# Performance work log

Hardware: AMD Instinct MI355X
Metric: run time of the kernel (lower is better)

The kernel has to match this reference:

```python
import jax, jax.numpy as jnp
import numpy as np

B, DIN, HID, DOUT, E, TOPK = 8192, 1024, 2048, 1024, 8, 2
GHID = HID // 2  # gating hidden


def setup_inputs() -> dict:
    key = jax.random.key(0)
    ks = jax.random.split(key, 16)
    s = lambda fan_in: 1.0 / np.sqrt(fan_in)
    return {
        "x": jax.random.normal(ks[0], (B, DIN), dtype=jnp.float32),
        # stacked expert params, leading axis = expert
        "w1": jax.random.uniform(ks[1], (E, DIN, HID), jnp.float32, -s(DIN), s(DIN)),
        "b1": jax.random.uniform(ks[2], (E, HID), jnp.float32, -s(DIN), s(DIN)),
        "w2": jax.random.uniform(ks[3], (E, HID, HID), jnp.float32, -s(HID), s(HID)),
        "b2": jax.random.uniform(ks[4], (E, HID), jnp.float32, -s(HID), s(HID)),
        "w3": jax.random.uniform(ks[5], (E, HID, DOUT), jnp.float32, -s(HID), s(HID)),
        "b3": jax.random.uniform(ks[6], (E, DOUT), jnp.float32, -s(HID), s(HID)),
        "wp": jax.random.uniform(ks[7], (E, DIN, HID), jnp.float32, -s(DIN), s(DIN)),
        "bp": jax.random.uniform(ks[8], (E, HID), jnp.float32, -s(DIN), s(DIN)),
        # gating network: Linear(DIN, GHID) -> ReLU -> Linear(GHID, E)
        "gw1": jax.random.uniform(ks[9], (DIN, GHID), jnp.float32, -s(DIN), s(DIN)),
        "gb1": jax.random.uniform(ks[10], (GHID,), jnp.float32, -s(DIN), s(DIN)),
        "gw2": jax.random.uniform(ks[11], (GHID, E), jnp.float32, -s(GHID), s(GHID)),
        "gb2": jax.random.uniform(ks[12], (E,), jnp.float32, -s(GHID), s(GHID)),
    }


def reference(x, w1, b1, w2, b2, w3, b3, wp, bp, gw1, gb1, gw2, gb2):
    # gating: [B, E]
    gate_logits = jnp.maximum(x @ gw1 + gb1, 0.0) @ gw2 + gb2
    topk_w, topk_i = jax.lax.top_k(gate_logits, TOPK)  # [B, K]
    topk_w = jax.nn.softmax(topk_w, axis=1)
    # dense per-expert residual MLP (dropout is identity in eval mode)
    h = jnp.maximum(jnp.einsum('bi,eih->beh', x, w1) + b1, 0.0)  # [B,E,HID]
    out = jnp.einsum('beh,ehg->beg', h, w2) + b2                  # [B,E,HID]
    identity = jnp.einsum('bi,eih->beh', x, wp) + bp              # projection
    out = jnp.maximum(out + identity, 0.0)
    expert_out = jnp.einsum('beh,eho->beo', out, w3) + b3         # [B,E,DOUT]
    # scatter top-k weights into dense [B, E] gate
    gate = jnp.zeros_like(gate_logits).at[jnp.arange(x.shape[0])[:, None], topk_i].set(topk_w)
    return jnp.einsum('beo,be->bo', expert_out, gate)             # [B, DOUT]
```

## Files before the change

### kernel.cpp

```cpp
#include <hip/hip_runtime.h>
#include <hip/hip_bf16.h>
#include <cstdint>
#include <cstddef>

#define TOK  8192
#define DIN  1024
#define HID  2048
#define DOUTN 1024
#define NEXP 8
#define GHID 1024

typedef __attribute__((ext_vector_type(8))) short bf16x8;
typedef __attribute__((ext_vector_type(4))) float floatx4;
typedef __attribute__((ext_vector_type(8))) unsigned short ushort8v;

__device__ __forceinline__ unsigned short f2b(float f) {
  unsigned int u = __float_as_uint(f);
  u += 0x7fffu + ((u >> 16) & 1u);
  return (unsigned short)(u >> 16);
}

__device__ __forceinline__ float b2f(unsigned short b) {
  return __uint_as_float(((unsigned int)b) << 16);
}

__device__ __forceinline__ void async_cp16(const unsigned short* g, char* lds) {
  __builtin_amdgcn_global_load_lds(
      (const __attribute__((address_space(1))) unsigned int*)g,
      (__attribute__((address_space(3))) unsigned int*)lds, 16, 0, 0);
}


__global__ void cvt_x_kernel(const float* __restrict__ src,
                             unsigned short* __restrict__ xb,
                             unsigned short* __restrict__ xcat, int n4) {
  int i = blockIdx.x * blockDim.x + threadIdx.x;
  if (i >= n4) return;
  float4 v = ((const float4*)src)[i];
  ushort4 hi, lo;
  hi.x = f2b(v.x); lo.x = f2b(v.x - b2f(hi.x));
  hi.y = f2b(v.y); lo.y = f2b(v.y - b2f(hi.y));
  hi.z = f2b(v.z); lo.z = f2b(v.z - b2f(hi.z));
  hi.w = f2b(v.w); lo.w = f2b(v.w - b2f(hi.w));
  ((ushort4*)xb)[i] = hi;
  int t = i >> 8;
  int kk = i & 255;
  ushort4* rowc = (ushort4*)(xcat + (size_t)t * 3072);
  rowc[kk] = hi;
  rowc[256 + kk] = hi;
  rowc[512 + kk] = lo;
}

__global__ void cvt_transpose_v2(const float* __restrict__ src,
                                 unsigned short* __restrict__ dst, int N,
                                 long sEstride, long dEstride, int ldDst) {
  __shared__ __align__(16) unsigned short t[64][72];
  long e = blockIdx.z;
  src += e * sEstride;
  dst += e * dEstride;
  int n0 = blockIdx.x * 64, k0 = blockIdx.y * 64;
  int tid = threadIdx.x;
  int kr = tid >> 2, qc = tid & 3;
  const float* s = src + (long)(k0 + kr) * N + n0 + qc * 16;
#pragma unroll
  for (int i = 0; i < 4; i++) {
    float4 v = *(const float4*)(s + i * 4);
    int nn = qc * 16 + i * 4;
    t[nn + 0][kr] = f2b(v.x);
    t[nn + 1][kr] = f2b(v.y);
    t[nn + 2][kr] = f2b(v.z);
    t[nn + 3][kr] = f2b(v.w);
  }
  __syncthreads();
  int c = tid & 7;
  int nr = tid >> 3;
#pragma unroll
  for (int p = 0; p < 2; p++) {
    int n = nr + 32 * p;
    ushort8v v = *(const ushort8v*)&t[n][c * 8];
    *(ushort8v*)(dst + (long)(n0 + n) * ldDst + k0 + c * 8) = v;
  }
}

__global__ void cvt_gw1_kernel(const float* __restrict__ src,
                               unsigned short* __restrict__ dst) {
  __shared__ float tile[32][33];
  int n0 = blockIdx.x * 32, k0 = blockIdx.y * 32;
  int x = threadIdx.x, y = threadIdx.y;
#pragma unroll
  for (int i = 0; i < 4; i++)
    tile[y + 8 * i][x] = src[(long)(k0 + y + 8 * i) * GHID + n0 + x];
  __syncthreads();
#pragma unroll
  for (int i = 0; i < 4; i++) {
    float v = tile[x][y + 8 * i];
    unsigned short hi = f2b(v);
    unsigned short lo = f2b(v - b2f(hi));
    size_t r = (size_t)(n0 + y + 8 * i) * 3072 + k0 + x;
    dst[r] = hi;
    dst[r + 1024] = lo;
    dst[r + 2048] = hi;
  }
}


#define KLOOP(pa0, pa1, pb0, pb1, NKT)                                        \
  for (int kt = 0; kt < (NKT); ++kt) {                                        \
    __syncthreads();                                                          \
    async_cp16((pa0) + kt * 32, ldsA0);                                       \
    async_cp16((pa1) + kt * 32, ldsA0 + 4096);                                \
    async_cp16((pb0) + kt * 32, ldsB0);                                       \
    async_cp16((pb1) + kt * 32, ldsB0 + 4096);                                \
    __syncthreads();                                                          \
    bf16x8 af[4], bfr[4];                                                     \
    _Pragma("unroll") for (int i = 0; i < 4; i++) {                           \
      af[i] = *(const bf16x8*)(AsB + i * 1024);                               \
      bfr[i] = *(const bf16x8*)(BsB + i * 1024);                              \
    }                                                                         \
    _Pragma("unroll") for (int mi = 0; mi < 4; mi++)                          \
      _Pragma("unroll") for (int ni = 0; ni < 4; ni++)                        \
        acc[mi][ni] = __builtin_amdgcn_mfma_f32_16x16x32_bf16(                \
            af[mi], bfr[ni], acc[mi][ni], 0, 0, 0);                           \
  }

#define TILE_SETUP()                                                          \
  int tid = threadIdx.x;                                                      \
  int sr = tid >> 2;                                                          \
  int lchunk = (tid & 3) ^ ((sr >> 1) & 3);                                   \
  int koffA = lchunk * 8;                                                     \
  char* ldsA0 = (char*)As + (tid & 192) * 16;                                 \
  char* ldsB0 = (char*)Bs + (tid & 192) * 16;                                 \
  int lane = tid & 63, wv = tid >> 6;                                         \
  int wm = (wv >> 1) << 6, wn = (wv & 1) << 6;                                \
  int q = lane >> 4, l15 = lane & 15;                                         \
  int abase = l15 * 64 + ((q ^ ((l15 >> 1) & 3)) << 4);                       \
  const char* AsB = (const char*)As + wm * 64 + abase;                        \
  const char* BsB = (const char*)Bs + wn * 64 + abase;                        \
  floatx4 acc[4][4] = {};


__global__ __launch_bounds__(256, 4) void gating_mfma(
    const unsigned short* __restrict__ xcat,
    const unsigned short* __restrict__ gw1t3,
    const float* __restrict__ gb1, float* __restrict__ H) {
  __shared__ __align__(16) unsigned short As[128 * 32];
  __shared__ __align__(16) unsigned short Bs[128 * 32];
  TILE_SETUP();
  int row0 = blockIdx.y << 7, tn = blockIdx.x << 7;

  const unsigned short* a0p = xcat + (size_t)(row0 + sr) * 3072 + koffA;
  const unsigned short* a1p = xcat + (size_t)(row0 + 64 + sr) * 3072 + koffA;
  const unsigned short* b0p = gw1t3 + (size_t)(tn + sr) * 3072 + koffA;
  const unsigned short* b1p = gw1t3 + (size_t)(tn + 64 + sr) * 3072 + koffA;

  KLOOP(a0p, a1p, b0p, b1p, 3072 / 32);

  int crow = row0 + wm + q * 4;
  int ccol0 = tn + wn + l15;
#pragma unroll
  for (int ni = 0; ni < 4; ++ni) {
    int col = ccol0 + ni * 16;
    float bias = gb1[col];
#pragma unroll
    for (int mi = 0; mi < 4; ++mi)
#pragma unroll
      for (int rg = 0; rg < 4; ++rg) {
        int rr = crow + mi * 16 + rg;
        H[(size_t)rr * GHID + col] = fmaxf(acc[mi][ni][rg] + bias, 0.f);
      }
  }
}


__global__ void gating2_topk(const float* __restrict__ H,
                             const float* __restrict__ gw2,
                             const float* __restrict__ gb2,
                             int* __restrict__ gidx, float* __restrict__ gwt) {
  int wv = threadIdx.x >> 6, lane = threadIdx.x & 63;
  int t = blockIdx.x * 4 + wv;
  const float* hrow = H + (size_t)t * GHID;
  float acc[8] = {};
  for (int k = lane; k < GHID; k += 64) {
    float v = hrow[k];
    float4 g0 = *(const float4*)(gw2 + (size_t)k * 8);
    float4 g1 = *(const float4*)(gw2 + (size_t)k * 8 + 4);
    acc[0] += v * g0.x; acc[1] += v * g0.y; acc[2] += v * g0.z; acc[3] += v * g0.w;
    acc[4] += v * g1.x; acc[5] += v * g1.y; acc[6] += v * g1.z; acc[7] += v * g1.w;
  }
#pragma unroll
  for (int off = 32; off > 0; off >>= 1)
#pragma unroll
    for (int e = 0; e < 8; e++) acc[e] += __shfl_xor(acc[e], off);

  if (lane == 0) {
    float l[8];
#pragma unroll
    for (int e = 0; e < 8; e++) l[e] = acc[e] + gb2[e];
    int b0 = 0; float v0 = l[0];
#pragma unroll
    for (int e = 1; e < 8; e++) if (l[e] > v0) { v0 = l[e]; b0 = e; }
    int b1 = -1; float v1 = -3.4e38f;
#pragma unroll
    for (int e = 0; e < 8; e++)
      if (e != b0 && l[e] > v1) { v1 = l[e]; b1 = e; }
    float ex = expf(v1 - v0);
    float inv = 1.f / (1.f + ex);
    gidx[2 * t] = b0; gidx[2 * t + 1] = b1;
    gwt[2 * t] = inv; gwt[2 * t + 1] = ex * inv;
  }
}


__global__ void route_count(const int* __restrict__ gidx, int* cnt) {
  int t = blockIdx.x * blockDim.x + threadIdx.x;
  int lane = threadIdx.x & 63;
  int e0 = gidx[2 * t], e1 = gidx[2 * t + 1];
#pragma unroll 1
  for (int e = 0; e < NEXP; e++) {
    unsigned long long m0 = __ballot(e0 == e);
    if (m0 && lane == __ffsll(m0) - 1) atomicAdd(&cnt[e], (int)__popcll(m0));
    unsigned long long m1 = __ballot(e1 == e);
    if (m1 && lane == __ffsll(m1) - 1) atomicAdd(&cnt[e], (int)__popcll(m1));
  }
}

__global__ void route_scan(const int* __restrict__ cnt, int* base_, int* cur) {
  if (threadIdx.x == 0) {
    int s = 0;
    for (int e = 0; e < NEXP; e++) { base_[e] = s; cur[e] = s; s += cnt[e]; }
  }
}

__global__ void route_scatter(const int* __restrict__ gidx,
                              const float* __restrict__ gwt, int* cur,
                              int* __restrict__ rt, float* __restrict__ rw,
                              int* __restrict__ inv) {
  int t = blockIdx.x * blockDim.x + threadIdx.x;
  int lane = threadIdx.x & 63;
  int e0 = gidx[2 * t], e1 = gidx[2 * t + 1];
  float w0 = gwt[2 * t], w1 = gwt[2 * t + 1];
#pragma unroll 1
  for (int e = 0; e < NEXP; e++) {
#pragma unroll 1
    for (int s = 0; s < 2; s++) {
      int mye = s ? e1 : e0;
      unsigned long long m = __ballot(mye == e);
      if (m) {
        int leader = __ffsll(m) - 1;
        int bb = 0;
        if (lane == leader) bb = atomicAdd(&cur[e], (int)__popcll(m));
        bb = __shfl(bb, leader);
        if (mye == e) {
          int pos = bb + (int)__popcll(m & ((1ull << lane) - 1ull));
          rt[pos] = t;
          rw[pos] = s ? w1 : w0;
          inv[2 * t + s] = pos;
        }
      }
    }
  }
}

__global__ void xgather_kernel(const unsigned short* __restrict__ xb,
                               const int* __restrict__ rt,
                               unsigned short* __restrict__ hx) {
  int slot = blockIdx.x;
  int c = threadIdx.x;
  int t = rt[slot];
  ((ushort8v*)(hx + (size_t)slot * 3072 + 2048))[c] =
      ((const ushort8v*)(xb + (size_t)t * 1024))[c];
}

__global__ void combine_kernel(const float* __restrict__ s3,
                               const int* __restrict__ inv,
                               float* __restrict__ out) {
  int t = blockIdx.x;
  int c = threadIdx.x;
  const float4* r0 = (const float4*)(s3 + (size_t)inv[2 * t] * DOUTN);
  const float4* r1 = (const float4*)(s3 + (size_t)inv[2 * t + 1] * DOUTN);
  float4 a = r0[c], b = r1[c];
  float4 o = {a.x + b.x, a.y + b.y, a.z + b.z, a.w + b.w};
  ((float4*)(out + (size_t)t * DOUTN))[c] = o;
}


#define STG_AU(dst, u, ktI)                                                   \
  async_cp16(Abase + aOff[u] + (size_t)(ktI) * 64, (dst) + (u) * 8192 + wvb)
#define STG_BU(dst, u, ktI)                                                   \
  async_cp16(Bbase + bOff[u] + (size_t)(ktI) * 64, (dst) + (u) * 8192 + wvb)

#define LDA8(dst, baseA, h)                                                   \
  _Pragma("unroll") for (int mi = 0; mi < 4; ++mi)                            \
      _Pragma("unroll") for (int kk = 0; kk < 2; ++kk)                        \
          (dst)[mi * 2 + kk] = *(const bf16x8*)(                              \
              (baseA) + ((wmo + (h)*64 + mi * 16 + l15) * 128 +               \
                         ((s0 ^ (kk << 2)) * 16)));

#define LDB4(dst, baseB, ch)                                                  \
  _Pragma("unroll") for (int ni = 0; ni < 2; ++ni)                            \
      _Pragma("unroll") for (int kk = 0; kk < 2; ++kk)                        \
          (dst)[ni * 2 + kk] = *(const bf16x8*)(                              \
              (baseB) + ((wno + (ch)*32 + ni * 16 + l15) * 128 +              \
                         ((s0 ^ (kk << 2)) * 16)));

#define MM8(aF, bF, mo, no)                                                   \
  _Pragma("unroll") for (int mi = 0; mi < 4; ++mi)                            \
      _Pragma("unroll") for (int ni = 0; ni < 2; ++ni)                        \
          _Pragma("unroll") for (int kk = 0; kk < 2; ++kk)                    \
              acc[(mo) + mi][(no) + ni] =                                     \
                  __builtin_amdgcn_mfma_f32_16x16x32_bf16(                    \
                      (aF)[mi * 2 + kk], (bF)[ni * 2 + kk],                   \
                      acc[(mo) + mi][(no) + ni], 0, 0, 0);


template <int MODE>
__global__ __launch_bounds__(512, 2) void moe_gemm8(
    const unsigned short* __restrict__ hx, const unsigned short* __restrict__ obuf,
    const unsigned short* __restrict__ w1t, const unsigned short* __restrict__ w2p,
    const unsigned short* __restrict__ w3t, const float* __restrict__ b1,
    const float* __restrict__ b2, const float* __restrict__ bp,
    const float* __restrict__ b3, const float* __restrict__ rw,
    const int* __restrict__ cnt, const int* __restrict__ basep,
    unsigned short* __restrict__ hxout, unsigned short* __restrict__ oout,
    float* __restrict__ s3) {
  __shared__ __align__(16) char smem[131072];

  const int gx = (int)gridDim.x;
  const int nwg = gx * (int)gridDim.y;
  int orig = (int)blockIdx.y * gx + (int)blockIdx.x;
  int q8 = nwg >> 3, r8 = nwg & 7;
  int xcd = orig & 7, loc = orig >> 3;
  int wg = (xcd < r8 ? xcd * (q8 + 1) : r8 * (q8 + 1) + (xcd - r8) * q8) + loc;
  int bx = wg % gx, by = wg / gx;

  int lt = by;
  int e, cn = 0, ok = 0;
  for (e = 0; e < NEXP; ++e) {
    int c = cnt[e];
    int nt = (c + 255) >> 8;
    if (lt < nt) { cn = c; ok = 1; break; }
    lt -= nt;
  }
  if (!ok) return;
  const int be = basep[e];
  const int row0 = lt << 8;
  const int tn = bx << 8;
  const int cnm1 = cn - 1;

  const int tid = threadIdx.x;
  const int lane = tid & 63, wv = tid >> 6;
  const int wmo = (wv >> 2) * 128;
  const int wno = (wv & 3) * 64;
  const int q = lane >> 4, l15 = lane & 15;
  const int s0 = q ^ (l15 & 7);
  const int wvb = wv * 1024;
  const int srow = tid >> 3;
  const int skoff = ((tid & 7) ^ (srow & 7)) * 8;

  const unsigned short* Abase;
  const unsigned short* Bbase;
  size_t strideA, strideB;
  if (MODE == 1) {
    Abase = hx + 2048; strideA = 3072;
    Bbase = w1t + (size_t)e * HID * DIN; strideB = DIN;
  } else if (MODE == 2) {
    Abase = hx; strideA = 3072;
    Bbase = w2p + (size_t)e * HID * 3072; strideB = 3072;
  } else {
    Abase = obuf; strideA = HID;
    Bbase = w3t + (size_t)e * DOUTN * HID; strideB = HID;
  }
  const int NT = (MODE == 1) ? (DIN / 64) : (MODE == 2 ? (3072 / 64) : (HID / 64));

  size_t aOff[4], bOff[4];
#pragma unroll
  for (int u = 0; u < 4; ++u) {
    int ra = min(row0 + u * 64 + srow, cnm1);
    aOff[u] = (size_t)(be + ra) * strideA + skoff;
    bOff[u] = (size_t)(tn + u * 64 + srow) * strideB + skoff;
  }

  char* const A0s = smem;
  char* const B0s = smem + 32768;
  char* const A1s = smem + 65536;
  char* const B1s = smem + 98304;

  floatx4 acc[8][4] = {};
  bf16x8 a[8], bA[4], bB[4];

  STG_AU(A0s, 0, 0); STG_AU(A0s, 1, 0); STG_AU(A0s, 2, 0); STG_AU(A0s, 3, 0);
  STG_BU(B0s, 0, 0); STG_BU(B0s, 1, 0); STG_BU(B0s, 2, 0); STG_BU(B0s, 3, 0);
  asm volatile("s_waitcnt vmcnt(4)" ::: "memory");
  STG_AU(A1s, 0, 1); STG_AU(A1s, 2, 1);
  STG_BU(B1s, 0, 1); STG_BU(B1s, 1, 1);
  STG_AU(A1s, 1, 1); STG_AU(A1s, 3, 1);
  asm volatile("s_waitcnt vmcnt(6)" ::: "memory");
  __builtin_amdgcn_s_barrier();

  for (int t = 0; t < NT; ++t) {
    char* const curA = (t & 1) ? A1s : A0s;
    char* const curB = (t & 1) ? B1s : B0s;
    char* const nxtB = (t & 1) ? B0s : B1s;
    LDA8(a, curA, 0);
    LDB4(bA, curB, 0);
    if (t + 1 < NT) { STG_BU(nxtB, 2, t + 1); STG_BU(nxtB, 3, t + 1); }
    __builtin_amdgcn_s_barrier();
    asm volatile("s_waitcnt lgkmcnt(0)" ::: "memory");
    __builtin_amdgcn_s_setprio(1);
    MM8(a, bA, 0, 0);
    __builtin_amdgcn_s_setprio(0);
    __builtin_amdgcn_s_barrier();
    LDB4(bB, curB, 1);
    if (t + 2 < NT) { STG_AU(curA, 0, t + 2); STG_AU(curA, 2, t + 2); }
    __builtin_amdgcn_s_barrier();
    asm volatile("s_waitcnt lgkmcnt(0)" ::: "memory");
    __builtin_amdgcn_s_setprio(1);
    MM8(a, bB, 0, 2);
    __builtin_amdgcn_s_setprio(0);
    __builtin_amdgcn_s_barrier();
    LDA8(a, curA, 1);
    if (t + 2 < NT) { STG_BU(curB, 0, t + 2); STG_BU(curB, 1, t + 2); }
    __builtin_amdgcn_s_barrier();
    asm volatile("s_waitcnt lgkmcnt(0)" ::: "memory");
    __builtin_amdgcn_s_setprio(1);
    MM8(a, bB, 4, 2);
    __builtin_amdgcn_s_setprio(0);
    __builtin_amdgcn_s_barrier();
    if (t + 2 < NT) {
      STG_AU(curA, 1, t + 2); STG_AU(curA, 3, t + 2);
      __builtin_amdgcn_s_setprio(1);
      MM8(a, bA, 4, 0);
      __builtin_amdgcn_s_setprio(0);
      asm volatile("s_waitcnt vmcnt(6)" ::: "memory");
    } else {
      __builtin_amdgcn_s_setprio(1);
      MM8(a, bA, 4, 0);
      __builtin_amdgcn_s_setprio(0);
      asm volatile("s_waitcnt vmcnt(0)" ::: "memory");
    }
    __builtin_amdgcn_s_barrier();
  }

  const int crow = row0 + wmo + q * 4;
  const int ccol0 = tn + wno + l15;
  if (MODE == 1) {
    const float* bb = b1 + (size_t)e * HID;
    float bias[4];
#pragma unroll
    for (int ni = 0; ni < 4; ++ni) bias[ni] = bb[ccol0 + ni * 16];
#pragma unroll
    for (int mi = 0; mi < 8; ++mi)
#pragma unroll
      for (int rg = 0; rg < 4; ++rg) {
        int rr = crow + mi * 16 + rg;
        if (rr < cn) {
#pragma unroll
          for (int ni = 0; ni < 4; ++ni)
            hxout[(size_t)(be + rr) * 3072 + ccol0 + ni * 16] =
                f2b(fmaxf(acc[mi][ni][rg] + bias[ni], 0.f));
        }
      }
  } else if (MODE == 2) {
    const float* bb = b2 + (size_t)e * HID;
    const float* bq = bp + (size_t)e * HID;
    float bias[4];
#pragma unroll
    for (int ni = 0; ni < 4; ++ni)
      bias[ni] = bb[ccol0 + ni * 16] + bq[ccol0 + ni * 16];
#pragma unroll
    for (int mi = 0; mi < 8; ++mi)
#pragma unroll
      for (int rg = 0; rg < 4; ++rg) {
        int rr = crow + mi * 16 + rg;
        if (rr < cn) {
#pragma unroll
          for (int ni = 0; ni < 4; ++ni)
            oout[(size_t)(be + rr) * HID + ccol0 + ni * 16] =
                f2b(fmaxf(acc[mi][ni][rg] + bias[ni], 0.f));
        }
      }
  } else {
    const float* bb = b3 + (size_t)e * DOUTN;
    float bias[4];
#pragma unroll
    for (int ni = 0; ni < 4; ++ni) bias[ni] = bb[ccol0 + ni * 16];
#pragma unroll
    for (int mi = 0; mi < 8; ++mi)
#pragma unroll
      for (int rg = 0; rg < 4; ++rg) {
        int rr = crow + mi * 16 + rg;
        if (rr < cn) {
          float wgt = rw[be + rr];
#pragma unroll
          for (int ni = 0; ni < 4; ++ni)
            s3[(size_t)(be + rr) * DOUTN + ccol0 + ni * 16] =
                (acc[mi][ni][rg] + bias[ni]) * wgt;
        }
      }
  }
}


extern "C" void kernel_launch(void* const* d_in, const int* in_sizes, int n_in,
                              void* d_out, int out_size, void* d_ws,
                              size_t ws_size, hipStream_t stream) {
  const float* x = (const float*)d_in[0];
  const float* w1 = (const float*)d_in[1];
  const float* b1 = (const float*)d_in[2];
  const float* w2 = (const float*)d_in[3];
  const float* b2 = (const float*)d_in[4];
  const float* w3 = (const float*)d_in[5];
  const float* b3 = (const float*)d_in[6];
  const float* wp = (const float*)d_in[7];
  const float* bp = (const float*)d_in[8];
  const float* gw1 = (const float*)d_in[9];
  const float* gb1 = (const float*)d_in[10];
  const float* gw2 = (const float*)d_in[11];
  const float* gb2 = (const float*)d_in[12];
  float* outp = (float*)d_out;
  char* ws = (char*)d_ws;

  const size_t o_w2p = 0;
  const size_t o_w3t = o_w2p + (size_t)NEXP * HID * 3072 * 2;
  const size_t o_xb  = o_w3t + (size_t)NEXP * DOUTN * HID * 2;
  const size_t o_w1t = o_xb + (size_t)TOK * DIN * 2;
  const size_t o_hg  = o_w1t + (size_t)NEXP * HID * DIN * 2;
  const size_t o_hx  = o_hg + (size_t)TOK * GHID * 4;
  const size_t o_gw1t3 = o_hx + (size_t)2 * TOK * 3072 * 2;
  const size_t o_gidx = o_gw1t3 + (size_t)GHID * 3072 * 2;
  const size_t o_gw  = o_gidx + (size_t)2 * TOK * 4;
  const size_t o_cnt = o_gw + (size_t)2 * TOK * 4;
  const size_t o_base = o_cnt + 128;
  const size_t o_cur = o_base + 128;
  const size_t o_rt  = o_cur + 128;
  const size_t o_rw  = o_rt + (size_t)2 * TOK * 4;
  const size_t o_inv = o_rw + (size_t)2 * TOK * 4;
  const size_t o_xcat = o_hx;
  const size_t o_ob   = o_w1t;
  const size_t o_s3   = o_w2p;

  unsigned short* w2p = (unsigned short*)(ws + o_w2p);
  unsigned short* w3t = (unsigned short*)(ws + o_w3t);
  unsigned short* xb = (unsigned short*)(ws + o_xb);
  unsigned short* w1t = (unsigned short*)(ws + o_w1t);
  float* hg = (float*)(ws + o_hg);
  unsigned short* hx = (unsigned short*)(ws + o_hx);
  unsigned short* gw1t3 = (unsigned short*)(ws + o_gw1t3);
  unsigned short* xcat = (unsigned short*)(ws + o_xcat);
  unsigned short* obuf = (unsigned short*)(ws + o_ob);
  float* s3 = (float*)(ws + o_s3);
  int* gidx = (int*)(ws + o_gidx);
  float* gwt = (float*)(ws + o_gw);
  int* cnt = (int*)(ws + o_cnt);
  int* basep = (int*)(ws + o_base);
  int* cur = (int*)(ws + o_cur);
  int* rtl = (int*)(ws + o_rt);
  float* rwl = (float*)(ws + o_rw);
  int* invp = (int*)(ws + o_inv);

  hipMemsetAsync(ws + o_cnt, 0, 32, stream);

  cvt_x_kernel<<<dim3(TOK * DIN / 4 / 256), 256, 0, stream>>>(x, xb, xcat, TOK * DIN / 4);
  cvt_gw1_kernel<<<dim3(GHID / 32, DIN / 32), dim3(32, 8), 0, stream>>>(gw1, gw1t3);
  cvt_transpose_v2<<<dim3(HID / 64, DIN / 64, NEXP), 256, 0, stream>>>(
      w1, w1t, HID, (long)DIN * HID, (long)HID * DIN, DIN);
  cvt_transpose_v2<<<dim3(HID / 64, HID / 64, NEXP), 256, 0, stream>>>(
      w2, w2p, HID, (long)HID * HID, (long)HID * 3072, 3072);
  cvt_transpose_v2<<<dim3(HID / 64, DIN / 64, NEXP), 256, 0, stream>>>(
      wp, w2p + 2048, HID, (long)DIN * HID, (long)HID * 3072, 3072);
  cvt_transpose_v2<<<dim3(DOUTN / 64, HID / 64, NEXP), 256, 0, stream>>>(
      w3, w3t, DOUTN, (long)HID * DOUTN, (long)DOUTN * HID, HID);

  gating_mfma<<<dim3(GHID / 128, TOK / 128), 256, 0, stream>>>(xcat, gw1t3, gb1, hg);
  gating2_topk<<<dim3(TOK / 4), 256, 0, stream>>>(hg, gw2, gb2, gidx, gwt);
  route_count<<<dim3(TOK / 256), 256, 0, stream>>>(gidx, cnt);
  route_scan<<<1, 64, 0, stream>>>(cnt, basep, cur);
  route_scatter<<<dim3(TOK / 256), 256, 0, stream>>>(gidx, gwt, cur, rtl, rwl, invp);
  xgather_kernel<<<dim3(2 * TOK), 128, 0, stream>>>(xb, rtl, hx);

  moe_gemm8<1><<<dim3(HID / 256, 71), 512, 0, stream>>>(
      hx, obuf, w1t, w2p, w3t, b1, b2, bp, b3, rwl, cnt, basep, hx, obuf, s3);
  moe_gemm8<2><<<dim3(HID / 256, 71), 512, 0, stream>>>(
      hx, obuf, w1t, w2p, w3t, b1, b2, bp, b3, rwl, cnt, basep, hx, obuf, s3);
  moe_gemm8<3><<<dim3(DOUTN / 256, 71), 512, 0, stream>>>(
      hx, obuf, w1t, w2p, w3t, b1, b2, bp, b3, rwl, cnt, basep, hx, obuf, s3);

  combine_kernel<<<dim3(TOK), 256, 0, stream>>>(s3, invp, outp);
}
```

Before: 1.033 ms.

## Route gating GEMM through moe_gemm8 with split-K and split-K the final expert GEMM

Removes the separate 128x128 gating GEMM kernel and runs the gating first layer through the larger 256x256 moe_gemm8 tile path (new MODE 0), split into two K halves whose partial sums are written to separate buffers. Bias and ReLU are moved into gating2_topk, which now sums the two partials. The third expert GEMM (MODE 3) is also split-K by two to add more workgroups, with the second partial added in combine_kernel. In exchange there is extra fp32 partial-buffer traffic and more buffer aliasing in the workspace.

```diff
diff --git a/kernel.cpp b/kernel.cpp
--- a/kernel.cpp
+++ b/kernel.cpp
@@ -104,84 +104,19 @@
 }
 
 
-#define KLOOP(pa0, pa1, pb0, pb1, NKT)                                        \
-  for (int kt = 0; kt < (NKT); ++kt) {                                        \
-    __syncthreads();                                                          \
-    async_cp16((pa0) + kt * 32, ldsA0);                                       \
-    async_cp16((pa1) + kt * 32, ldsA0 + 4096);                                \
-    async_cp16((pb0) + kt * 32, ldsB0);                                       \
-    async_cp16((pb1) + kt * 32, ldsB0 + 4096);                                \
-    __syncthreads();                                                          \
-    bf16x8 af[4], bfr[4];                                                     \
-    _Pragma("unroll") for (int i = 0; i < 4; i++) {                           \
-      af[i] = *(const bf16x8*)(AsB + i * 1024);                               \
-      bfr[i] = *(const bf16x8*)(BsB + i * 1024);                              \
-    }                                                                         \
-    _Pragma("unroll") for (int mi = 0; mi < 4; mi++)                          \
-      _Pragma("unroll") for (int ni = 0; ni < 4; ni++)                        \
-        acc[mi][ni] = __builtin_amdgcn_mfma_f32_16x16x32_bf16(                \
-            af[mi], bfr[ni], acc[mi][ni], 0, 0, 0);                           \
-  }
-
-#define TILE_SETUP()                                                          \
-  int tid = threadIdx.x;                                                      \
-  int sr = tid >> 2;                                                          \
-  int lchunk = (tid & 3) ^ ((sr >> 1) & 3);                                   \
-  int koffA = lchunk * 8;                                                     \
-  char* ldsA0 = (char*)As + (tid & 192) * 16;                                 \
-  char* ldsB0 = (char*)Bs + (tid & 192) * 16;                                 \
-  int lane = tid & 63, wv = tid >> 6;                                         \
-  int wm = (wv >> 1) << 6, wn = (wv & 1) << 6;                                \
-  int q = lane >> 4, l15 = lane & 15;                                         \
-  int abase = l15 * 64 + ((q ^ ((l15 >> 1) & 3)) << 4);                       \
-  const char* AsB = (const char*)As + wm * 64 + abase;                        \
-  const char* BsB = (const char*)Bs + wn * 64 + abase;                        \
-  floatx4 acc[4][4] = {};
-
-
-__global__ __launch_bounds__(256, 4) void gating_mfma(
-    const unsigned short* __restrict__ xcat,
-    const unsigned short* __restrict__ gw1t3,
-    const float* __restrict__ gb1, float* __restrict__ H) {
-  __shared__ __align__(16) unsigned short As[128 * 32];
-  __shared__ __align__(16) unsigned short Bs[128 * 32];
-  TILE_SETUP();
-  int row0 = blockIdx.y << 7, tn = blockIdx.x << 7;
-
-  const unsigned short* a0p = xcat + (size_t)(row0 + sr) * 3072 + koffA;
-  const unsigned short* a1p = xcat + (size_t)(row0 + 64 + sr) * 3072 + koffA;
-  const unsigned short* b0p = gw1t3 + (size_t)(tn + sr) * 3072 + koffA;
-  const unsigned short* b1p = gw1t3 + (size_t)(tn + 64 + sr) * 3072 + koffA;
-
-  KLOOP(a0p, a1p, b0p, b1p, 3072 / 32);
-
-  int crow = row0 + wm + q * 4;
-  int ccol0 = tn + wn + l15;
-#pragma unroll
-  for (int ni = 0; ni < 4; ++ni) {
-    int col = ccol0 + ni * 16;
-    float bias = gb1[col];
-#pragma unroll
-    for (int mi = 0; mi < 4; ++mi)
-#pragma unroll
-      for (int rg = 0; rg < 4; ++rg) {
-        int rr = crow + mi * 16 + rg;
-        H[(size_t)rr * GHID + col] = fmaxf(acc[mi][ni][rg] + bias, 0.f);
-      }
-  }
-}
-
-
-__global__ void gating2_topk(const float* __restrict__ H,
+__global__ void gating2_topk(const float* __restrict__ H0,
+                             const float* __restrict__ H1,
+                             const float* __restrict__ gb1,
                              const float* __restrict__ gw2,
                              const float* __restrict__ gb2,
                              int* __restrict__ gidx, float* __restrict__ gwt) {
   int wv = threadIdx.x >> 6, lane = threadIdx.x & 63;
   int t = blockIdx.x * 4 + wv;
-  const float* hrow = H + (size_t)t * GHID;
+  const float* h0 = H0 + (size_t)t * GHID;
+  const float* h1 = H1 + (size_t)t * GHID;
   float acc[8] = {};
   for (int k = lane; k < GHID; k += 64) {
-    float v = hrow[k];
+    float v = fmaxf(h0[k] + h1[k] + gb1[k], 0.f);
     float4 g0 = *(const float4*)(gw2 + (size_t)k * 8);
     float4 g1 = *(const float4*)(gw2 + (size_t)k * 8 + 4);
     acc[0] += v * g0.x; acc[1] += v * g0.y; acc[2] += v * g0.z; acc[3] += v * g0.w;
@@ -272,14 +207,18 @@
 }
 
 __global__ void combine_kernel(const float* __restrict__ s3,
+                               const float* __restrict__ s3b,
                                const int* __restrict__ inv,
                                float* __restrict__ out) {
   int t = blockIdx.x;
   int c = threadIdx.x;
-  const float4* r0 = (const float4*)(s3 + (size_t)inv[2 * t] * DOUTN);
-  const float4* r1 = (const float4*)(s3 + (size_t)inv[2 * t + 1] * DOUTN);
-  float4 a = r0[c], b = r1[c];
-  float4 o = {a.x + b.x, a.y + b.y, a.z + b.z, a.w + b.w};
+  int i0 = inv[2 * t], i1 = inv[2 * t + 1];
+  float4 a = ((const float4*)(s3 + (size_t)i0 * DOUTN))[c];
+  float4 b = ((const float4*)(s3 + (size_t)i1 * DOUTN))[c];
+  float4 a2 = ((const float4*)(s3b + (size_t)i0 * DOUTN))[c];
+  float4 b2 = ((const float4*)(s3b + (size_t)i1 * DOUTN))[c];
+  float4 o = {a.x + b.x + a2.x + b2.x, a.y + b.y + a2.y + b2.y,
+              a.z + b.z + a2.z + b2.z, a.w + b.w + a2.w + b2.w};
   ((float4*)(out + (size_t)t * DOUTN))[c] = o;
 }
 
@@ -312,38 +251,43 @@
                       (aF)[mi * 2 + kk], (bF)[ni * 2 + kk],                   \
                       acc[(mo) + mi][(no) + ni], 0, 0, 0);
 
-
 template <int MODE>
 __global__ __launch_bounds__(512, 2) void moe_gemm8(
     const unsigned short* __restrict__ hx, const unsigned short* __restrict__ obuf,
     const unsigned short* __restrict__ w1t, const unsigned short* __restrict__ w2p,
-    const unsigned short* __restrict__ w3t, const float* __restrict__ b1,
+    const unsigned short* __restrict__ w3t, const unsigned short* __restrict__ xcat,
+    const unsigned short* __restrict__ gw1t3, const float* __restrict__ b1,
     const float* __restrict__ b2, const float* __restrict__ bp,
     const float* __restrict__ b3, const float* __restrict__ rw,
     const int* __restrict__ cnt, const int* __restrict__ basep,
     unsigned short* __restrict__ hxout, unsigned short* __restrict__ oout,
-    float* __restrict__ s3) {
+    float* __restrict__ s3, float* __restrict__ s3b,
+    float* __restrict__ hg0, float* __restrict__ hg1) {
   __shared__ __align__(16) char smem[131072];
 
-  const int gx = (int)gridDim.x;
-  const int nwg = gx * (int)gridDim.y;
+  const int gx = (int)gridDim.x, gy = (int)gridDim.y;
+  const int kz = (int)blockIdx.z;
+  const int nwg = gx * gy;
   int orig = (int)blockIdx.y * gx + (int)blockIdx.x;
   int q8 = nwg >> 3, r8 = nwg & 7;
   int xcd = orig & 7, loc = orig >> 3;
   int wg = (xcd < r8 ? xcd * (q8 + 1) : r8 * (q8 + 1) + (xcd - r8) * q8) + loc;
-  int bx = wg % gx, by = wg / gx;
-
-  int lt = by;
-  int e, cn = 0, ok = 0;
-  for (e = 0; e < NEXP; ++e) {
-    int c = cnt[e];
-    int nt = (c + 255) >> 8;
-    if (lt < nt) { cn = c; ok = 1; break; }
-    lt -= nt;
-  }
-  if (!ok) return;
-  const int be = basep[e];
-  const int row0 = lt << 8;
+  int by = wg % gy, bx = wg / gy;
+
+  int e = 0, cn = TOK, be = 0, row0 = by << 8;
+  if (MODE != 0) {
+    int lt = by, ok = 0;
+    cn = 0;
+    for (e = 0; e < NEXP; ++e) {
+      int c = cnt[e];
+      int nt = (c + 255) >> 8;
+      if (lt < nt) { cn = c; ok = 1; break; }
+      lt -= nt;
+    }
+    if (!ok) return;
+    be = basep[e];
+    row0 = lt << 8;
+  }
   const int tn = bx << 8;
   const int cnm1 = cn - 1;
 
@@ -360,17 +304,24 @@
   const unsigned short* Abase;
   const unsigned short* Bbase;
   size_t strideA, strideB;
-  if (MODE == 1) {
+  int NT;
+  if (MODE == 0) {
+    Abase = xcat + (size_t)kz * 1536; strideA = 3072;
+    Bbase = gw1t3 + (size_t)kz * 1536; strideB = 3072;
+    NT = 1536 / 64;
+  } else if (MODE == 1) {
     Abase = hx + 2048; strideA = 3072;
     Bbase = w1t + (size_t)e * HID * DIN; strideB = DIN;
+    NT = DIN / 64;
   } else if (MODE == 2) {
     Abase = hx; strideA = 3072;
     Bbase = w2p + (size_t)e * HID * 3072; strideB = 3072;
+    NT = 3072 / 64;
   } else {
-    Abase = obuf; strideA = HID;
-    Bbase = w3t + (size_t)e * DOUTN * HID; strideB = HID;
-  }
-  const int NT = (MODE == 1) ? (DIN / 64) : (MODE == 2 ? (3072 / 64) : (HID / 64));
+    Abase = obuf + (size_t)kz * 1024; strideA = HID;
+    Bbase = w3t + (size_t)e * DOUTN * HID + (size_t)kz * 1024; strideB = HID;
+    NT = 1024 / 64;
+  }
 
   size_t aOff[4], bOff[4];
 #pragma unroll
@@ -443,7 +394,18 @@
 
   const int crow = row0 + wmo + q * 4;
   const int ccol0 = tn + wno + l15;
-  if (MODE == 1) {
+  if (MODE == 0) {
+    float* Hp = kz ? hg1 : hg0;
+#pragma unroll
+    for (int mi = 0; mi < 8; ++mi)
+#pragma unroll
+      for (int rg = 0; rg < 4; ++rg) {
+        int rr = crow + mi * 16 + rg;
+#pragma unroll
+        for (int ni = 0; ni < 4; ++ni)
+          Hp[(size_t)rr * GHID + ccol0 + ni * 16] = acc[mi][ni][rg];
+      }
+  } else if (MODE == 1) {
     const float* bb = b1 + (size_t)e * HID;
     float bias[4];
 #pragma unroll
@@ -481,9 +443,11 @@
       }
   } else {
     const float* bb = b3 + (size_t)e * DOUTN;
+    float* dst = kz ? s3b : s3;
     float bias[4];
 #pragma unroll
-    for (int ni = 0; ni < 4; ++ni) bias[ni] = bb[ccol0 + ni * 16];
+    for (int ni = 0; ni < 4; ++ni)
+      bias[ni] = kz ? 0.f : bb[ccol0 + ni * 16];
 #pragma unroll
     for (int mi = 0; mi < 8; ++mi)
 #pragma unroll
@@ -493,7 +457,7 @@
           float wgt = rw[be + rr];
 #pragma unroll
           for (int ni = 0; ni < 4; ++ni)
-            s3[(size_t)(be + rr) * DOUTN + ccol0 + ni * 16] =
+            dst[(size_t)(be + rr) * DOUTN + ccol0 + ni * 16] =
                 (acc[mi][ni][rg] + bias[ni]) * wgt;
         }
       }
@@ -536,19 +500,23 @@
   const size_t o_rw  = o_rt + (size_t)2 * TOK * 4;
   const size_t o_inv = o_rw + (size_t)2 * TOK * 4;
   const size_t o_xcat = o_hx;
+  const size_t o_hg2  = o_hx + (size_t)TOK * 3072 * 2;
   const size_t o_ob   = o_w1t;
   const size_t o_s3   = o_w2p;
+  const size_t o_s3b  = o_hx;
 
   unsigned short* w2p = (unsigned short*)(ws + o_w2p);
   unsigned short* w3t = (unsigned short*)(ws + o_w3t);
   unsigned short* xb = (unsigned short*)(ws + o_xb);
   unsigned short* w1t = (unsigned short*)(ws + o_w1t);
   float* hg = (float*)(ws + o_hg);
+  float* hg2 = (float*)(ws + o_hg2);
   unsigned short* hx = (unsigned short*)(ws + o_hx);
   unsigned short* gw1t3 = (unsigned short*)(ws + o_gw1t3);
   unsigned short* xcat = (unsigned short*)(ws + o_xcat);
   unsigned short* obuf = (unsigned short*)(ws + o_ob);
   float* s3 = (float*)(ws + o_s3);
+  float* s3b = (float*)(ws + o_s3b);
   int* gidx = (int*)(ws + o_gidx);
   float* gwt = (float*)(ws + o_gw);
   int* cnt = (int*)(ws + o_cnt);
@@ -571,19 +539,24 @@
   cvt_transpose_v2<<<dim3(DOUTN / 64, HID / 64, NEXP), 256, 0, stream>>>(
       w3, w3t, DOUTN, (long)HID * DOUTN, (long)DOUTN * HID, HID);
 
-  gating_mfma<<<dim3(GHID / 128, TOK / 128), 256, 0, stream>>>(xcat, gw1t3, gb1, hg);
-  gating2_topk<<<dim3(TOK / 4), 256, 0, stream>>>(hg, gw2, gb2, gidx, gwt);
+  moe_gemm8<0><<<dim3(GHID / 256, TOK / 256, 2), 512, 0, stream>>>(
+      hx, obuf, w1t, w2p, w3t, xcat, gw1t3, b1, b2, bp, b3, rwl, cnt, basep,
+      hx, obuf, s3, s3b, hg, hg2);
+  gating2_topk<<<dim3(TOK / 4), 256, 0, stream>>>(hg, hg2, gb1, gw2, gb2, gidx, gwt);
   route_count<<<dim3(TOK / 256), 256, 0, stream>>>(gidx, cnt);
   route_scan<<<1, 64, 0, stream>>>(cnt, basep, cur);
   route_scatter<<<dim3(TOK / 256), 256, 0, stream>>>(gidx, gwt, cur, rtl, rwl, invp);
   xgather_kernel<<<dim3(2 * TOK), 128, 0, stream>>>(xb, rtl, hx);
 
   moe_gemm8<1><<<dim3(HID / 256, 71), 512, 0, stream>>>(
-      hx, obuf, w1t, w2p, w3t, b1, b2, bp, b3, rwl, cnt, basep, hx, obuf, s3);
+      hx, obuf, w1t, w2p, w3t, xcat, gw1t3, b1, b2, bp, b3, rwl, cnt, basep,
+      hx, obuf, s3, s3b, hg, hg2);
   moe_gemm8<2><<<dim3(HID / 256, 71), 512, 0, stream>>>(
-      hx, obuf, w1t, w2p, w3t, b1, b2, bp, b3, rwl, cnt, basep, hx, obuf, s3);
-  moe_gemm8<3><<<dim3(DOUTN / 256, 71), 512, 0, stream>>>(
-      hx, obuf, w1t, w2p, w3t, b1, b2, bp, b3, rwl, cnt, basep, hx, obuf, s3);
-
-  combine_kernel<<<dim3(TOK), 256, 0, stream>>>(s3, invp, outp);
-}
+      hx, obuf, w1t, w2p, w3t, xcat, gw1t3, b1, b2, bp, b3, rwl, cnt, basep,
+      hx, obuf, s3, s3b, hg, hg2);
+  moe_gemm8<3><<<dim3(DOUTN / 256, 71, 2), 512, 0, stream>>>(
+      hx, obuf, w1t, w2p, w3t, xcat, gw1t3, b1, b2, bp, b3, rwl, cnt, basep,
+      hx, obuf, s3, s3b, hg, hg2);
+
+  combine_kernel<<<dim3(TOK), 256, 0, stream>>>(s3, s3b, invp, outp);
+}
```

Result: no change. 1.015 ms (-1.8%).
